# Performance work log

Hardware: AMD Instinct MI355X
Metric: run time of the kernel (lower is better)

Reference implementation:

```python
import jax, jax.numpy as jnp
import numpy as np

IN_F, OUT_F = 4096, 4096
IN_Q, OUT_Q = IN_F // 4, OUT_F // 4


def setup_inputs() -> dict:
    key = jax.random.key(0)
    kx, kr, ki, kj, kk = jax.random.split(key, 5)
    std = 1.0 / np.sqrt(IN_F)
    x = jax.random.normal(kx, (4, 2048, IN_F), dtype=jnp.float32)
    Wr = std * jax.random.normal(kr, (OUT_Q, IN_Q), dtype=jnp.float32)
    Wi = std * jax.random.normal(ki, (OUT_Q, IN_Q), dtype=jnp.float32)
    Wj = std * jax.random.normal(kj, (OUT_Q, IN_Q), dtype=jnp.float32)
    Wk = std * jax.random.normal(kk, (OUT_Q, IN_Q), dtype=jnp.float32)
    bias = jnp.zeros((OUT_F,), dtype=jnp.float32)
    return {"x": x, "Wr": Wr, "Wi": Wi, "Wj": Wj, "Wk": Wk, "bias": bias}


def _hamilton_block(Wr, Wi, Wj, Wk):
    # Assemble the structured [4*out_q, 4*in_q] Hamilton block weight so the
    # whole op is ONE large GEMM instead of 16 small ones (same math).
    row_r = jnp.concatenate([Wr, -Wi, -Wj, -Wk], axis=1)
    row_i = jnp.concatenate([Wi,  Wr,  Wk, -Wj], axis=1)
    row_j = jnp.concatenate([Wj, -Wk,  Wr,  Wi], axis=1)
    row_k = jnp.concatenate([Wk,  Wj, -Wi,  Wr], axis=1)
    return jnp.concatenate([row_r, row_i, row_j, row_k], axis=0)  # [OUT_F, IN_F]


def reference(x, Wr, Wi, Wj, Wk, bias):
    W = _hamilton_block(Wr, Wi, Wj, Wk)
    # x: [B, S, IN_F] @ W.T -> [B, S, OUT_F]
    out = jnp.einsum('bsf,of->bso', x, W) + bias
    return out
```

## Files before the change

### kernel.cpp

```cpp
#include <hip/hip_runtime.h>
#include <hip/hip_bf16.h>


#define M_DIM 8192
#define N_DIM 4096
#define K_DIM 4096
#define BK 64
#define NT (K_DIM / BK)

typedef __attribute__((ext_vector_type(8))) short bf16x8;
typedef __attribute__((ext_vector_type(4))) float f32x4;
typedef __attribute__((ext_vector_type(16))) float f32x16;
typedef __attribute__((ext_vector_type(8))) unsigned short ushort8;

static __device__ __forceinline__ unsigned short f2bf(float f) {
    unsigned int u = __float_as_uint(f);
    return (unsigned short)((u + 0x7fffu + ((u >> 16) & 1u)) >> 16);
}
static __device__ __forceinline__ unsigned short f2bf_sgn(float f, unsigned int sg) {
    unsigned int u = __float_as_uint(f) ^ sg;
    return (unsigned short)((u + 0x7fffu + ((u >> 16) & 1u)) >> 16);
}

__global__ __launch_bounds__(256) void cvt_x_kernel(const float* __restrict__ x,
                                                    unsigned short* __restrict__ xb) {
    int i = (blockIdx.x * 256 + threadIdx.x) * 8;
    f32x4 a = __builtin_nontemporal_load((const f32x4*)(x + i));
    f32x4 b = __builtin_nontemporal_load((const f32x4*)(x + i + 4));
    ushort8 o;
    o[0] = f2bf(a[0]); o[1] = f2bf(a[1]); o[2] = f2bf(a[2]); o[3] = f2bf(a[3]);
    o[4] = f2bf(b[0]); o[5] = f2bf(b[1]); o[6] = f2bf(b[2]); o[7] = f2bf(b[3]);
    *(ushort8*)(xb + i) = o;
}

__global__ __launch_bounds__(256) void prep_w_kernel(const float* __restrict__ Wr,
    const float* __restrict__ Wi, const float* __restrict__ Wj,
    const float* __restrict__ Wk, unsigned short* __restrict__ wb) {
    int row = blockIdx.x >> 1;
    int col = ((blockIdx.x & 1) * 256 + threadIdx.x) * 8;
    int p = row >> 10, q = col >> 10;
    int ci = p ^ q;
    const float* src = (ci == 0) ? Wr : (ci == 1) ? Wi : (ci == 2) ? Wj : Wk;
    unsigned int sg = ((0x428Eu >> (p * 4 + q)) & 1u) << 31;
    int so = (row & 1023) * 1024 + (col & 1023);
    f32x4 a = *(const f32x4*)(src + so);
    f32x4 b = *(const f32x4*)(src + so + 4);
    ushort8 o;
    o[0] = f2bf_sgn(a[0], sg); o[1] = f2bf_sgn(a[1], sg);
    o[2] = f2bf_sgn(a[2], sg); o[3] = f2bf_sgn(a[3], sg);
    o[4] = f2bf_sgn(b[0], sg); o[5] = f2bf_sgn(b[1], sg);
    o[6] = f2bf_sgn(b[2], sg); o[7] = f2bf_sgn(b[3], sg);
    *(ushort8*)(wb + row * 4096 + col) = o;
}

#define GLD16(gp, lp) __builtin_amdgcn_global_load_lds( \
    (const __attribute__((address_space(1))) void*)(gp), \
    (__attribute__((address_space(3))) void*)(lp), 16, 0, 0)

#define BAR() do { asm volatile("" ::: "memory"); \
                   __builtin_amdgcn_s_barrier(); \
                   asm volatile("" ::: "memory"); } while (0)
#define VM0() asm volatile("s_waitcnt vmcnt(0)" ::: "memory")
#define SB()  __builtin_amdgcn_sched_barrier(0)
#define LGKM(n) do { asm volatile("s_waitcnt lgkmcnt(" #n ")" ::: "memory"); SB(); } while (0)

#define DSR(dst, addr, imm) \
    asm volatile("ds_read_b128 %0, %1 offset:" imm : "=v"(dst) : "v"(addr))

#define MF32(a, b, c) __builtin_amdgcn_mfma_f32_32x32x16_bf16(a, b, c, 0, 0, 0)

#define DECL6(F) bf16x8 F##a0, F##a1, F##a2, F##a3, F##b0, F##b1
#define RD6(F, A0, A1, A2, A3, B0, B1) do { \
    DSR(F##a0, vA, A0); DSR(F##a1, vA, A1); DSR(F##a2, vA, A2); DSR(F##a3, vA, A3); \
    DSR(F##b0, vB, B0); DSR(F##b1, vB, B1); } while (0)

#define MFMA8(F) do { \
    __builtin_amdgcn_s_setprio(1); \
    acc[0][0] = MF32(F##a0, F##b0, acc[0][0]); \
    acc[0][1] = MF32(F##a0, F##b1, acc[0][1]); \
    acc[1][0] = MF32(F##a1, F##b0, acc[1][0]); \
    acc[1][1] = MF32(F##a1, F##b1, acc[1][1]); \
    acc[2][0] = MF32(F##a2, F##b0, acc[2][0]); \
    acc[2][1] = MF32(F##a2, F##b1, acc[2][1]); \
    acc[3][0] = MF32(F##a3, F##b0, acc[3][0]); \
    acc[3][1] = MF32(F##a3, F##b1, acc[3][1]); \
    __builtin_amdgcn_s_setprio(0); \
} while (0)

__global__ __launch_bounds__(512, 2) void qgemm_bf16(
    const unsigned short* __restrict__ A, const unsigned short* __restrict__ B,
    const float* __restrict__ bias, float* __restrict__ out)
{
    __shared__ __align__(16) unsigned short Lsh[65536];

    int bid = blockIdx.x;
    int cpx = gridDim.x >> 3;
    int wg  = (bid & 7) * cpx + (bid >> 3);
    int brow = (wg >> 4) * 256;
    int bcol = (wg & 15) * 256;

    int tid  = threadIdx.x;
    int lane = tid & 63;
    int wid  = tid >> 6;
    int wm   = wid >> 2;
    int wn   = wid & 3;
    int l31  = lane & 31;
    int hi   = lane >> 5;

    const unsigned short* Ag = A + (size_t)brow * K_DIM;
    const unsigned short* Bg = B + (size_t)bcol * K_DIM;

    unsigned lds0 = (unsigned)(size_t)(__attribute__((address_space(3))) void*)Lsh;
    unsigned vA = lds0 + (unsigned)(wm * 4096 + l31 * 32 + hi * 16);
    unsigned vB = lds0 + 32768u + (unsigned)(wn * 2048 + l31 * 32 + hi * 16);

    int soff[4];
    #pragma unroll
    for (int i = 0; i < 4; ++i) {
        int c = i * 512 + tid;
        soff[i] = ((c >> 1) & 255) * 4096 + (c >> 9) * 16 + (c & 1) * 8;
    }

    f32x16 acc[4][2] = {};

    auto STAGE = [&](int buf, int t) {
        const unsigned short* ga = Ag + t * BK;
        const unsigned short* gb = Bg + t * BK;
        char* l = (char*)Lsh + buf * 65536;
        #pragma unroll
        for (int i = 0; i < 4; ++i)
            GLD16(ga + soff[i], l + (i * 512 + tid) * 16);
        #pragma unroll
        for (int i = 0; i < 4; ++i)
            GLD16(gb + soff[i], l + 32768 + (i * 512 + tid) * 16);
    };

    STAGE(0, 0);
    VM0(); BAR();

    for (int t = 0; t < NT; ++t) {
        if (t + 1 < NT) STAGE((t & 1) ^ 1, t + 1);

        DECL6(f0); DECL6(f1); DECL6(f2); DECL6(f3);
        RD6(f0, "0", "1024", "2048", "3072", "0", "1024");
        RD6(f1, "8192", "9216", "10240", "11264", "8192", "9216");
        LGKM(6);
        MFMA8(f0);
        RD6(f2, "16384", "17408", "18432", "19456", "16384", "17408");
        LGKM(6);
        MFMA8(f1);
        RD6(f3, "24576", "25600", "26624", "27648", "24576", "25600");
        LGKM(6);
        MFMA8(f2);
        LGKM(0);
        MFMA8(f3);

        VM0();
        BAR();
        vA ^= 0x10000u; vB ^= 0x10000u;
    }

    #pragma unroll
    for (int ni = 0; ni < 2; ++ni) {
        int col = bcol + wn * 64 + ni * 32 + l31;
        float bv = bias[col];
        #pragma unroll
        for (int mi = 0; mi < 4; ++mi) {
            int r0 = brow + wm * 128 + mi * 32 + 4 * hi;
            #pragma unroll
            for (int r = 0; r < 16; ++r) {
                int row = r0 + (r & 3) + 8 * (r >> 2);
                __builtin_nontemporal_store(acc[mi][ni][r] + bv,
                                            &out[(size_t)row * N_DIM + col]);
            }
        }
    }
}

#define FBM 128
#define FBN 128
#define FBK 64
__global__ __launch_bounds__(256) void qgemm_fb(const float* __restrict__ x,
    const float* __restrict__ Wr, const float* __restrict__ Wi,
    const float* __restrict__ Wj, const float* __restrict__ Wk,
    const float* __restrict__ bias, float* __restrict__ out)
{
    __shared__ unsigned short As[FBM * FBK];
    __shared__ unsigned short Bs[FBN * FBK];

    int bid = blockIdx.x;
    int cpx = gridDim.x >> 3;
    int wg = (bid & 7) * cpx + (bid >> 3);
    int brow = (wg >> 5) * FBM;
    int bcol = (wg & 31) * FBN;

    int tid = threadIdx.x;
    int lane = tid & 63;
    int wv = tid >> 6;
    int wm = (wv >> 1) << 6;
    int wn = (wv & 1) << 6;
    int fr = lane & 15;
    int fk = (lane >> 4) << 3;

    int p = bcol >> 10;
    f32x4 acc[4][4] = {};

    for (int kt = 0; kt < K_DIM / FBK; ++kt) {
        int k0 = kt * FBK;
        int q = k0 >> 10;
        int ci = p ^ q;
        const float* wsrc = (ci == 0) ? Wr : (ci == 1) ? Wi : (ci == 2) ? Wj : Wk;
        unsigned int sg = ((0x428Eu >> (p * 4 + q)) & 1u) << 31;

        __syncthreads();
        #pragma unroll
        for (int i = 0; i < 4; ++i) {
            int c = i * 256 + tid;
            int row = c >> 3, colo = (c & 7) << 3;
            const float* s = x + (size_t)(brow + row) * K_DIM + k0 + colo;
            float4 a = *(const float4*)s;
            float4 b = *(const float4*)(s + 4);
            ushort8 o;
            o[0] = f2bf(a.x); o[1] = f2bf(a.y); o[2] = f2bf(a.z); o[3] = f2bf(a.w);
            o[4] = f2bf(b.x); o[5] = f2bf(b.y); o[6] = f2bf(b.z); o[7] = f2bf(b.w);
            *(ushort8*)(&As[c << 3]) = o;
        }
        #pragma unroll
        for (int i = 0; i < 4; ++i) {
            int c = i * 256 + tid;
            int row = c >> 3, colo = (c & 7) << 3;
            const float* s = wsrc + ((bcol + row) & 1023) * 1024 + ((k0 + colo) & 1023);
            float4 a = *(const float4*)s;
            float4 b = *(const float4*)(s + 4);
            ushort8 o;
            o[0] = f2bf_sgn(a.x, sg); o[1] = f2bf_sgn(a.y, sg);
            o[2] = f2bf_sgn(a.z, sg); o[3] = f2bf_sgn(a.w, sg);
            o[4] = f2bf_sgn(b.x, sg); o[5] = f2bf_sgn(b.y, sg);
            o[6] = f2bf_sgn(b.z, sg); o[7] = f2bf_sgn(b.w, sg);
            *(ushort8*)(&Bs[c << 3]) = o;
        }
        __syncthreads();

        #pragma unroll
        for (int ks = 0; ks < 2; ++ks) {
            bf16x8 af[4], bfr[4];
            #pragma unroll
            for (int m = 0; m < 4; ++m)
                af[m] = *(const bf16x8*)(&As[(wm + m * 16 + fr) * FBK + ks * 32 + fk]);
            #pragma unroll
            for (int n = 0; n < 4; ++n)
                bfr[n] = *(const bf16x8*)(&Bs[(wn + n * 16 + fr) * FBK + ks * 32 + fk]);
            #pragma unroll
            for (int m = 0; m < 4; ++m)
                #pragma unroll
                for (int n = 0; n < 4; ++n)
                    acc[m][n] = __builtin_amdgcn_mfma_f32_16x16x32_bf16(
                        af[m], bfr[n], acc[m][n], 0, 0, 0);
        }
    }

    int cr = (lane >> 4) << 2;
    int cc = lane & 15;
    #pragma unroll
    for (int n = 0; n < 4; ++n) {
        int col = bcol + wn + n * 16 + cc;
        float bv = bias[col];
        #pragma unroll
        for (int m = 0; m < 4; ++m) {
            int r0 = brow + wm + m * 16 + cr;
            #pragma unroll
            for (int r = 0; r < 4; ++r)
                out[(size_t)(r0 + r) * N_DIM + col] = acc[m][n][r] + bv;
        }
    }
}

extern "C" void kernel_launch(void* const* d_in, const int* in_sizes, int n_in,
                              void* d_out, int out_size, void* d_ws, size_t ws_size,
                              hipStream_t stream) {
    const float* x    = (const float*)d_in[0];
    const float* Wr   = (const float*)d_in[1];
    const float* Wi   = (const float*)d_in[2];
    const float* Wj   = (const float*)d_in[3];
    const float* Wk   = (const float*)d_in[4];
    const float* bias = (const float*)d_in[5];
    float* out = (float*)d_out;

    const size_t xb_bytes = (size_t)M_DIM * K_DIM * 2;
    const size_t wb_bytes = (size_t)N_DIM * K_DIM * 2;

    if (ws_size >= xb_bytes + wb_bytes) {
        unsigned short* xb = (unsigned short*)d_ws;
        unsigned short* wb = (unsigned short*)((char*)d_ws + xb_bytes);
        cvt_x_kernel<<<(M_DIM * K_DIM) / 2048, 256, 0, stream>>>(x, xb);
        prep_w_kernel<<<N_DIM * 2, 256, 0, stream>>>(Wr, Wi, Wj, Wk, wb);
        const int n_blocks = (M_DIM / 256) * (N_DIM / 256);
        qgemm_bf16<<<n_blocks, 512, 0, stream>>>(xb, wb, bias, out);
    } else {
        const int n_blocks = (M_DIM / FBM) * (N_DIM / FBN);
        qgemm_fb<<<n_blocks, 256, 0, stream>>>(x, Wr, Wi, Wj, Wk, bias, out);
    }
}
```

Baseline: 311.0 us.

## Switch LDS tile layout to row-major with XOR swizzle for conflict-free reads

Changes the shared-memory layout of the A and B tiles from a k-chunk-major arrangement to a row-major one (128 bytes per row), with 16-byte chunks XOR-swizzled by row index. Global-to-LDS load offsets and the per-lane ds_read addresses are recomputed to match, and the k-step is now selected by XORing the base address. The aim is to make global loads more contiguous per row and to cut LDS bank conflicts on the ds_read_b128 operand fetches. It adds per-read address XOR arithmetic, and the swizzle has to agree exactly on both the write and read sides.

```diff
diff --git a/kernel.cpp b/kernel.cpp
--- a/kernel.cpp
+++ b/kernel.cpp
@@ -70,9 +70,11 @@
 #define MF32(a, b, c) __builtin_amdgcn_mfma_f32_32x32x16_bf16(a, b, c, 0, 0, 0)
 
 #define DECL6(F) bf16x8 F##a0, F##a1, F##a2, F##a3, F##b0, F##b1
-#define RD6(F, A0, A1, A2, A3, B0, B1) do { \
-    DSR(F##a0, vA, A0); DSR(F##a1, vA, A1); DSR(F##a2, vA, A2); DSR(F##a3, vA, A3); \
-    DSR(F##b0, vB, B0); DSR(F##b1, vB, B1); } while (0)
+#define RD6(F, KX) do { \
+    unsigned aA_ = vA ^ (KX), aB_ = vB ^ (KX); \
+    DSR(F##a0, aA_, "0");     DSR(F##a1, aA_, "4096"); \
+    DSR(F##a2, aA_, "8192");  DSR(F##a3, aA_, "12288"); \
+    DSR(F##b0, aB_, "0");     DSR(F##b1, aB_, "4096"); } while (0)
 
 #define MFMA8(F) do { \
     __builtin_amdgcn_s_setprio(1); \
@@ -106,19 +108,23 @@
     int wn   = wid & 3;
     int l31  = lane & 31;
     int hi   = lane >> 5;
+    unsigned e0 = (unsigned)(l31 & 1);
+    unsigned e1 = (unsigned)((l31 >> 1) & 3);
 
     const unsigned short* Ag = A + (size_t)brow * K_DIM;
     const unsigned short* Bg = B + (size_t)bcol * K_DIM;
 
     unsigned lds0 = (unsigned)(size_t)(__attribute__((address_space(3))) void*)Lsh;
-    unsigned vA = lds0 + (unsigned)(wm * 4096 + l31 * 32 + hi * 16);
-    unsigned vB = lds0 + 32768u + (unsigned)(wn * 2048 + l31 * 32 + hi * 16);
+    unsigned vA = lds0 + (unsigned)(wm * 16384 + l31 * 128)
+                + (((unsigned)hi ^ e0) << 4) + (e1 << 5);
+    unsigned vB = lds0 + 32768u + (unsigned)(wn * 8192 + l31 * 128)
+                + (((unsigned)hi ^ e0) << 4) + (e1 << 5);
 
     int soff[4];
     #pragma unroll
     for (int i = 0; i < 4; ++i) {
         int c = i * 512 + tid;
-        soff[i] = ((c >> 1) & 255) * 4096 + (c >> 9) * 16 + (c & 1) * 8;
+        soff[i] = (c >> 3) * K_DIM + (((c & 7) ^ ((c >> 3) & 7)) << 3);
     }
 
     f32x16 acc[4][2] = {};
@@ -128,11 +134,10 @@
         const unsigned short* gb = Bg + t * BK;
         char* l = (char*)Lsh + buf * 65536;
         #pragma unroll
-        for (int i = 0; i < 4; ++i)
+        for (int i = 0; i < 4; ++i) {
             GLD16(ga + soff[i], l + (i * 512 + tid) * 16);
-        #pragma unroll
-        for (int i = 0; i < 4; ++i)
             GLD16(gb + soff[i], l + 32768 + (i * 512 + tid) * 16);
+        }
     };
 
     STAGE(0, 0);
@@ -142,14 +147,14 @@
         if (t + 1 < NT) STAGE((t & 1) ^ 1, t + 1);
 
         DECL6(f0); DECL6(f1); DECL6(f2); DECL6(f3);
-        RD6(f0, "0", "1024", "2048", "3072", "0", "1024");
-        RD6(f1, "8192", "9216", "10240", "11264", "8192", "9216");
+        RD6(f0, 0u);
+        RD6(f1, 32u);
         LGKM(6);
         MFMA8(f0);
-        RD6(f2, "16384", "17408", "18432", "19456", "16384", "17408");
+        RD6(f2, 64u);
         LGKM(6);
         MFMA8(f1);
-        RD6(f3, "24576", "25600", "26624", "27648", "24576", "25600");
+        RD6(f3, 96u);
         LGKM(6);
         MFMA8(f2);
         LGKM(0);
```

Measured after the change: 289.8 us. -6.8%, faster.

## Pre-swizzle X into MFMA fragment layout and load A directly to registers

Applied to the files above, without the earlier changes.

The X conversion kernel now transposes each 128x64 tile through shared memory and writes it into MFMA-operand order, so the GEMM can fetch A fragments straight into registers with global_load_dwordx4 and skip LDS for A. Only B is staged in LDS, now with an XOR swizzle and half the LDS footprint, and A loads run in a multi-stage register pipeline controlled by vmcnt waits. The goal is to cut LDS traffic and barrier pressure in the main loop. In exchange, A is no longer shared across waves: four waves reload the same A fragments from global/L2, which adds register pressure and global load traffic.

```diff
diff --git a/kernel.cpp b/kernel.cpp
--- a/kernel.cpp
+++ b/kernel.cpp
@@ -22,15 +22,31 @@
     return (unsigned short)((u + 0x7fffu + ((u >> 16) & 1u)) >> 16);
 }
 
-__global__ __launch_bounds__(256) void cvt_x_kernel(const float* __restrict__ x,
-                                                    unsigned short* __restrict__ xb) {
-    int i = (blockIdx.x * 256 + threadIdx.x) * 8;
-    f32x4 a = __builtin_nontemporal_load((const f32x4*)(x + i));
-    f32x4 b = __builtin_nontemporal_load((const f32x4*)(x + i + 4));
-    ushort8 o;
-    o[0] = f2bf(a[0]); o[1] = f2bf(a[1]); o[2] = f2bf(a[2]); o[3] = f2bf(a[3]);
-    o[4] = f2bf(b[0]); o[5] = f2bf(b[1]); o[6] = f2bf(b[2]); o[7] = f2bf(b[3]);
-    *(ushort8*)(xb + i) = o;
+__global__ __launch_bounds__(256) void cvt_x_t(const float* __restrict__ x,
+                                               unsigned short* __restrict__ xbt) {
+    __shared__ unsigned short T[128][72];
+    int bid = blockIdx.x;
+    int h = bid >> 6, t = bid & 63;
+    int tid = threadIdx.x;
+
+    #pragma unroll
+    for (int j = 0; j < 8; ++j) {
+        int c = j * 256 + tid;
+        int r = c >> 4, ko = (c & 15) * 4;
+        f32x4 v = __builtin_nontemporal_load(
+            (const f32x4*)(x + (size_t)(h * 128 + r) * 4096 + t * 64 + ko));
+        T[r][ko + 0] = f2bf(v[0]); T[r][ko + 1] = f2bf(v[1]);
+        T[r][ko + 2] = f2bf(v[2]); T[r][ko + 3] = f2bf(v[3]);
+    }
+    __syncthreads();
+    #pragma unroll
+    for (int i = 0; i < 4; ++i) {
+        int c = i * 256 + tid;
+        int ln = c & 63, mi = (c >> 6) & 3, kc = c >> 8;
+        int row = mi * 32 + (ln & 31), k = kc * 16 + (ln >> 5) * 8;
+        *(ushort8*)(xbt + (size_t)(h * 64 + t) * 8192 + (size_t)c * 8) =
+            *(const ushort8*)&T[row][k];
+    }
 }
 
 __global__ __launch_bounds__(256) void prep_w_kernel(const float* __restrict__ Wr,
@@ -60,113 +76,133 @@
 #define BAR() do { asm volatile("" ::: "memory"); \
                    __builtin_amdgcn_s_barrier(); \
                    asm volatile("" ::: "memory"); } while (0)
-#define VM0() asm volatile("s_waitcnt vmcnt(0)" ::: "memory")
 #define SB()  __builtin_amdgcn_sched_barrier(0)
-#define LGKM(n) do { asm volatile("s_waitcnt lgkmcnt(" #n ")" ::: "memory"); SB(); } while (0)
-
-#define DSR(dst, addr, imm) \
-    asm volatile("ds_read_b128 %0, %1 offset:" imm : "=v"(dst) : "v"(addr))
+#define VM(n) do { asm volatile("s_waitcnt vmcnt(" #n ")" ::: "memory"); SB(); } while (0)
 
 #define MF32(a, b, c) __builtin_amdgcn_mfma_f32_32x32x16_bf16(a, b, c, 0, 0, 0)
 
-#define DECL6(F) bf16x8 F##a0, F##a1, F##a2, F##a3, F##b0, F##b1
-#define RD6(F, A0, A1, A2, A3, B0, B1) do { \
-    DSR(F##a0, vA, A0); DSR(F##a1, vA, A1); DSR(F##a2, vA, A2); DSR(F##a3, vA, A3); \
-    DSR(F##b0, vB, B0); DSR(F##b1, vB, B1); } while (0)
-
-#define MFMA8(F) do { \
+#define ALOAD4(K, P) \
+    asm volatile("global_load_dwordx4 %0, %4, off\n\t" \
+                 "global_load_dwordx4 %1, %4, off offset:1024\n\t" \
+                 "global_load_dwordx4 %2, %4, off offset:2048\n\t" \
+                 "global_load_dwordx4 %3, %4, off offset:3072" \
+        : "=&v"(a##K##_0), "=&v"(a##K##_1), "=&v"(a##K##_2), "=&v"(a##K##_3) \
+        : "v"(P))
+
+#define MFMA8(A0, A1, A2, A3, B0, B1) do { \
     __builtin_amdgcn_s_setprio(1); \
-    acc[0][0] = MF32(F##a0, F##b0, acc[0][0]); \
-    acc[0][1] = MF32(F##a0, F##b1, acc[0][1]); \
-    acc[1][0] = MF32(F##a1, F##b0, acc[1][0]); \
-    acc[1][1] = MF32(F##a1, F##b1, acc[1][1]); \
-    acc[2][0] = MF32(F##a2, F##b0, acc[2][0]); \
-    acc[2][1] = MF32(F##a2, F##b1, acc[2][1]); \
-    acc[3][0] = MF32(F##a3, F##b0, acc[3][0]); \
-    acc[3][1] = MF32(F##a3, F##b1, acc[3][1]); \
+    acc[0][0] = MF32(A0, B0, acc[0][0]); acc[0][1] = MF32(A0, B1, acc[0][1]); \
+    acc[1][0] = MF32(A1, B0, acc[1][0]); acc[1][1] = MF32(A1, B1, acc[1][1]); \
+    acc[2][0] = MF32(A2, B0, acc[2][0]); acc[2][1] = MF32(A2, B1, acc[2][1]); \
+    acc[3][0] = MF32(A3, B0, acc[3][0]); acc[3][1] = MF32(A3, B1, acc[3][1]); \
     __builtin_amdgcn_s_setprio(0); \
+} while (0)
+
+#define BREAD(KC) \
+    bf16x8 b0 = *(const bf16x8*)(bb + (vB0 ^ ((KC) << 5))); \
+    bf16x8 b1 = *(const bf16x8*)(bb + (vB0 ^ ((KC) << 5)) + 4096)
+
+#define STAGEB(dstOff, tt) do { \
+    const unsigned short* gb_ = Bg + (tt) * BK; \
+    char* lb_ = (char*)Bsh + (dstOff); \
+    _Pragma("unroll") \
+    for (int i_ = 0; i_ < 4; ++i_) \
+        GLD16(gb_ + soffB[i_], lb_ + (i_ * 512 + tid) * 16); \
 } while (0)
 
 __global__ __launch_bounds__(512, 2) void qgemm_bf16(
     const unsigned short* __restrict__ A, const unsigned short* __restrict__ B,
     const float* __restrict__ bias, float* __restrict__ out)
 {
-    __shared__ __align__(16) unsigned short Lsh[65536];
+    __shared__ __align__(16) unsigned short Bsh[32768];
 
     int bid = blockIdx.x;
     int cpx = gridDim.x >> 3;
     int wg  = (bid & 7) * cpx + (bid >> 3);
-    int brow = (wg >> 4) * 256;
+    int mt   = wg >> 4;
     int bcol = (wg & 15) * 256;
 
     int tid  = threadIdx.x;
     int lane = tid & 63;
     int wid  = tid >> 6;
-    int wm   = wid >> 2;
+    int hA   = wid >> 2;
     int wn   = wid & 3;
     int l31  = lane & 31;
     int hi   = lane >> 5;
 
-    const unsigned short* Ag = A + (size_t)brow * K_DIM;
+    const char* pA0 = (const char*)A
+        + (size_t)((mt * 2 + hA) * 64) * 16384 + lane * 16;
+    const char* pA1 = pA0 + 4096;
+    const char* pA2 = pA0 + 8192;
+    const char* pA3 = pA0 + 12288;
+
     const unsigned short* Bg = B + (size_t)bcol * K_DIM;
-
-    unsigned lds0 = (unsigned)(size_t)(__attribute__((address_space(3))) void*)Lsh;
-    unsigned vA = lds0 + (unsigned)(wm * 4096 + l31 * 32 + hi * 16);
-    unsigned vB = lds0 + 32768u + (unsigned)(wn * 2048 + l31 * 32 + hi * 16);
-
-    int soff[4];
+    int soffB[4];
     #pragma unroll
     for (int i = 0; i < 4; ++i) {
         int c = i * 512 + tid;
-        soff[i] = ((c >> 1) & 255) * 4096 + (c >> 9) * 16 + (c & 1) * 8;
-    }
+        soffB[i] = (c >> 3) * K_DIM + (((c & 7) ^ ((c >> 3) & 7)) << 3);
+    }
+
+    unsigned vB0 = (unsigned)((wn * 64 + l31) * 128)
+                 + (((unsigned)hi ^ (unsigned)(l31 & 1)) << 4)
+                 + (((unsigned)(l31 >> 1) & 3u) << 5);
+    unsigned rb = 0;
 
     f32x16 acc[4][2] = {};
-
-    auto STAGE = [&](int buf, int t) {
-        const unsigned short* ga = Ag + t * BK;
-        const unsigned short* gb = Bg + t * BK;
-        char* l = (char*)Lsh + buf * 65536;
-        #pragma unroll
-        for (int i = 0; i < 4; ++i)
-            GLD16(ga + soff[i], l + (i * 512 + tid) * 16);
-        #pragma unroll
-        for (int i = 0; i < 4; ++i)
-            GLD16(gb + soff[i], l + 32768 + (i * 512 + tid) * 16);
-    };
-
-    STAGE(0, 0);
-    VM0(); BAR();
-
-    for (int t = 0; t < NT; ++t) {
-        if (t + 1 < NT) STAGE((t & 1) ^ 1, t + 1);
-
-        DECL6(f0); DECL6(f1); DECL6(f2); DECL6(f3);
-        RD6(f0, "0", "1024", "2048", "3072", "0", "1024");
-        RD6(f1, "8192", "9216", "10240", "11264", "8192", "9216");
-        LGKM(6);
-        MFMA8(f0);
-        RD6(f2, "16384", "17408", "18432", "19456", "16384", "17408");
-        LGKM(6);
-        MFMA8(f1);
-        RD6(f3, "24576", "25600", "26624", "27648", "24576", "25600");
-        LGKM(6);
-        MFMA8(f2);
-        LGKM(0);
-        MFMA8(f3);
-
-        VM0();
+    bf16x8 a0_0, a0_1, a0_2, a0_3;
+    bf16x8 a1_0, a1_1, a1_2, a1_3;
+    bf16x8 a2_0, a2_1, a2_2, a2_3;
+    bf16x8 a3_0, a3_1, a3_2, a3_3;
+
+    STAGEB(0, 0);
+    ALOAD4(0, pA0);
+    ALOAD4(1, pA1);
+
+    for (int t = 0; t < NT - 1; ++t) {
+        const char* bb = (const char*)Bsh + rb;
+        ALOAD4(2, pA2);
+        VM(8);
         BAR();
-        vA ^= 0x10000u; vB ^= 0x10000u;
-    }
-
+        { BREAD(0); MFMA8(a0_0, a0_1, a0_2, a0_3, b0, b1); }
+        ALOAD4(3, pA3);
+        STAGEB(rb ^ 0x8000u, t + 1);
+        VM(12);
+        { BREAD(1); MFMA8(a1_0, a1_1, a1_2, a1_3, b0, b1); }
+        pA0 += 16384;
+        ALOAD4(0, pA0);
+        VM(12);
+        { BREAD(2); MFMA8(a2_0, a2_1, a2_2, a2_3, b0, b1); }
+        pA1 += 16384;
+        ALOAD4(1, pA1);
+        pA2 += 16384; pA3 += 16384;
+        VM(12);
+        { BREAD(3); MFMA8(a3_0, a3_1, a3_2, a3_3, b0, b1); }
+        rb ^= 0x8000u;
+    }
+    {
+        const char* bb = (const char*)Bsh + rb;
+        ALOAD4(2, pA2);
+        VM(8);
+        BAR();
+        { BREAD(0); MFMA8(a0_0, a0_1, a0_2, a0_3, b0, b1); }
+        ALOAD4(3, pA3);
+        VM(8);
+        { BREAD(1); MFMA8(a1_0, a1_1, a1_2, a1_3, b0, b1); }
+        VM(4);
+        { BREAD(2); MFMA8(a2_0, a2_1, a2_2, a2_3, b0, b1); }
+        VM(0);
+        { BREAD(3); MFMA8(a3_0, a3_1, a3_2, a3_3, b0, b1); }
+    }
+
+    int brow = mt * 256;
     #pragma unroll
     for (int ni = 0; ni < 2; ++ni) {
         int col = bcol + wn * 64 + ni * 32 + l31;
         float bv = bias[col];
         #pragma unroll
         for (int mi = 0; mi < 4; ++mi) {
-            int r0 = brow + wm * 128 + mi * 32 + 4 * hi;
+            int r0 = brow + hA * 128 + mi * 32 + 4 * hi;
             #pragma unroll
             for (int r = 0; r < 16; ++r) {
                 int row = r0 + (r & 3) + 8 * (r >> 2);
@@ -290,12 +326,12 @@
     const size_t wb_bytes = (size_t)N_DIM * K_DIM * 2;
 
     if (ws_size >= xb_bytes + wb_bytes) {
-        unsigned short* xb = (unsigned short*)d_ws;
-        unsigned short* wb = (unsigned short*)((char*)d_ws + xb_bytes);
-        cvt_x_kernel<<<(M_DIM * K_DIM) / 2048, 256, 0, stream>>>(x, xb);
+        unsigned short* xbt = (unsigned short*)d_ws;
+        unsigned short* wb  = (unsigned short*)((char*)d_ws + xb_bytes);
+        cvt_x_t<<<64 * 64, 256, 0, stream>>>(x, xbt);
         prep_w_kernel<<<N_DIM * 2, 256, 0, stream>>>(Wr, Wi, Wj, Wk, wb);
         const int n_blocks = (M_DIM / 256) * (N_DIM / 256);
-        qgemm_bf16<<<n_blocks, 512, 0, stream>>>(xb, wb, bias, out);
+        qgemm_bf16<<<n_blocks, 512, 0, stream>>>(xbt, wb, bias, out);
     } else {
         const int n_blocks = (M_DIM / FBM) * (N_DIM / FBN);
         qgemm_fb<<<n_blocks, 256, 0, stream>>>(x, Wr, Wi, Wj, Wk, bias, out);
```

Result: faster. 291.3 us (-6.3%).

## Restructure bf16 GEMM main loop with swizzled LDS and split A/B prefetch

Applied to the files above, without the earlier changes.

Changes the LDS tile layout to row-major 128-byte rows with an XOR swizzle, which is meant to reduce ds_read bank conflicts. A and B halves are now loaded in separate stages, with B prefetched two iterations ahead and A one iteration ahead, interleaved with the MFMA clusters and a mid-iteration barrier. The hand-written inline asm ds_reads and explicit lgkmcnt waits are replaced by plain C++ loads, so instruction scheduling is left to the compiler. The partial vmcnt waits are intended to overlap global loads with compute. The cost is more complex buffer-reuse timing, which risks races and scheduling regressions.

```diff
diff --git a/kernel.cpp b/kernel.cpp
--- a/kernel.cpp
+++ b/kernel.cpp
@@ -60,38 +60,15 @@
 #define BAR() do { asm volatile("" ::: "memory"); \
                    __builtin_amdgcn_s_barrier(); \
                    asm volatile("" ::: "memory"); } while (0)
-#define VM0() asm volatile("s_waitcnt vmcnt(0)" ::: "memory")
-#define SB()  __builtin_amdgcn_sched_barrier(0)
-#define LGKM(n) do { asm volatile("s_waitcnt lgkmcnt(" #n ")" ::: "memory"); SB(); } while (0)
-
-#define DSR(dst, addr, imm) \
-    asm volatile("ds_read_b128 %0, %1 offset:" imm : "=v"(dst) : "v"(addr))
+#define VM(n) asm volatile("s_waitcnt vmcnt(" #n ")" ::: "memory")
 
 #define MF32(a, b, c) __builtin_amdgcn_mfma_f32_32x32x16_bf16(a, b, c, 0, 0, 0)
-
-#define DECL6(F) bf16x8 F##a0, F##a1, F##a2, F##a3, F##b0, F##b1
-#define RD6(F, A0, A1, A2, A3, B0, B1) do { \
-    DSR(F##a0, vA, A0); DSR(F##a1, vA, A1); DSR(F##a2, vA, A2); DSR(F##a3, vA, A3); \
-    DSR(F##b0, vB, B0); DSR(F##b1, vB, B1); } while (0)
-
-#define MFMA8(F) do { \
-    __builtin_amdgcn_s_setprio(1); \
-    acc[0][0] = MF32(F##a0, F##b0, acc[0][0]); \
-    acc[0][1] = MF32(F##a0, F##b1, acc[0][1]); \
-    acc[1][0] = MF32(F##a1, F##b0, acc[1][0]); \
-    acc[1][1] = MF32(F##a1, F##b1, acc[1][1]); \
-    acc[2][0] = MF32(F##a2, F##b0, acc[2][0]); \
-    acc[2][1] = MF32(F##a2, F##b1, acc[2][1]); \
-    acc[3][0] = MF32(F##a3, F##b0, acc[3][0]); \
-    acc[3][1] = MF32(F##a3, F##b1, acc[3][1]); \
-    __builtin_amdgcn_s_setprio(0); \
-} while (0)
 
 __global__ __launch_bounds__(512, 2) void qgemm_bf16(
     const unsigned short* __restrict__ A, const unsigned short* __restrict__ B,
     const float* __restrict__ bias, float* __restrict__ out)
 {
-    __shared__ __align__(16) unsigned short Lsh[65536];
+    __shared__ __align__(16) unsigned short Lsh[2][2][2][128 * 64];
 
     int bid = blockIdx.x;
     int cpx = gridDim.x >> 3;
@@ -102,63 +79,89 @@
     int tid  = threadIdx.x;
     int lane = tid & 63;
     int wid  = tid >> 6;
-    int wm   = wid >> 2;
+    int hA   = wid >> 2;
     int wn   = wid & 3;
+    int hB   = wn >> 1;
+    int rB0  = (wn & 1) << 6;
     int l31  = lane & 31;
     int hi   = lane >> 5;
 
     const unsigned short* Ag = A + (size_t)brow * K_DIM;
     const unsigned short* Bg = B + (size_t)bcol * K_DIM;
-
-    unsigned lds0 = (unsigned)(size_t)(__attribute__((address_space(3))) void*)Lsh;
-    unsigned vA = lds0 + (unsigned)(wm * 4096 + l31 * 32 + hi * 16);
-    unsigned vB = lds0 + 32768u + (unsigned)(wn * 2048 + l31 * 32 + hi * 16);
-
-    int soff[4];
-    #pragma unroll
-    for (int i = 0; i < 4; ++i) {
-        int c = i * 512 + tid;
-        soff[i] = ((c >> 1) & 255) * 4096 + (c >> 9) * 16 + (c & 1) * 8;
-    }
+    const char* LshB = (const char*)&Lsh[0][0][0][0];
+
+    unsigned inrow = (((unsigned)hi ^ (unsigned)(l31 & 1)) << 4)
+                   + (((unsigned)(l31 >> 1) & 3u) << 5);
+    unsigned oA = (unsigned)(hA * 16384 + l31 * 128) + inrow;
+    unsigned oB = 32768u + (unsigned)(hB * 16384 + (rB0 + l31) * 128) + inrow;
 
     f32x16 acc[4][2] = {};
 
-    auto STAGE = [&](int buf, int t) {
-        const unsigned short* ga = Ag + t * BK;
-        const unsigned short* gb = Bg + t * BK;
-        char* l = (char*)Lsh + buf * 65536;
-        #pragma unroll
-        for (int i = 0; i < 4; ++i)
-            GLD16(ga + soff[i], l + (i * 512 + tid) * 16);
-        #pragma unroll
-        for (int i = 0; i < 4; ++i)
-            GLD16(gb + soff[i], l + 32768 + (i * 512 + tid) * 16);
+    auto stage = [&](int buf, int ab, int half, int t) {
+        const unsigned short* g = (ab ? Bg : Ag) + (size_t)(half << 7) * K_DIM + t * BK;
+        unsigned short* l = &Lsh[buf][ab][half][0];
+        #pragma unroll
+        for (int i = 0; i < 2; ++i) {
+            int c = i * 512 + tid;
+            int r = c >> 3, s = c & 7;
+            GLD16(g + (size_t)r * K_DIM + ((s ^ (r & 7)) << 3), l + (c << 3));
+        }
     };
-
-    STAGE(0, 0);
-    VM0(); BAR();
+    auto RD = [&](unsigned off) -> bf16x8 {
+        return *(const bf16x8*)(LshB + off);
+    };
+
+#define CLUST(kc) do { \
+    __builtin_amdgcn_s_setprio(1); \
+    acc[0][0] = MF32(aF##kc##0, bA[kc], acc[0][0]); \
+    acc[0][1] = MF32(aF##kc##0, bB[kc], acc[0][1]); \
+    acc[1][0] = MF32(aF##kc##1, bA[kc], acc[1][0]); \
+    acc[1][1] = MF32(aF##kc##1, bB[kc], acc[1][1]); \
+    acc[2][0] = MF32(aF##kc##2, bA[kc], acc[2][0]); \
+    acc[2][1] = MF32(aF##kc##2, bB[kc], acc[2][1]); \
+    acc[3][0] = MF32(aF##kc##3, bA[kc], acc[3][0]); \
+    acc[3][1] = MF32(aF##kc##3, bB[kc], acc[3][1]); \
+    __builtin_amdgcn_s_setprio(0); \
+} while (0)
+
+#define RDA(kc) \
+    bf16x8 aF##kc##0 = RD((oA ^ ((unsigned)(kc) << 5))); \
+    bf16x8 aF##kc##1 = RD((oA ^ ((unsigned)(kc) << 5)) + 4096u); \
+    bf16x8 aF##kc##2 = RD((oA ^ ((unsigned)(kc) << 5)) + 8192u); \
+    bf16x8 aF##kc##3 = RD((oA ^ ((unsigned)(kc) << 5)) + 12288u)
+
+    stage(0, 0, 0, 0); stage(0, 0, 1, 0); stage(0, 1, 0, 0); stage(0, 1, 1, 0);
+    stage(1, 1, 0, 1); stage(1, 1, 1, 1);
+    VM(4); BAR();
 
     for (int t = 0; t < NT; ++t) {
-        if (t + 1 < NT) STAGE((t & 1) ^ 1, t + 1);
-
-        DECL6(f0); DECL6(f1); DECL6(f2); DECL6(f3);
-        RD6(f0, "0", "1024", "2048", "3072", "0", "1024");
-        RD6(f1, "8192", "9216", "10240", "11264", "8192", "9216");
-        LGKM(6);
-        MFMA8(f0);
-        RD6(f2, "16384", "17408", "18432", "19456", "16384", "17408");
-        LGKM(6);
-        MFMA8(f1);
-        RD6(f3, "24576", "25600", "26624", "27648", "24576", "25600");
-        LGKM(6);
-        MFMA8(f2);
-        LGKM(0);
-        MFMA8(f3);
-
-        VM0();
+        bf16x8 bA[4], bB[4];
+
+        #pragma unroll
+        for (int kc = 0; kc < 4; ++kc) {
+            unsigned ob = oB ^ ((unsigned)kc << 5);
+            bA[kc] = RD(ob);
+            bB[kc] = RD(ob + 4096u);
+        }
+        RDA(0);
+        if (t + 1 < NT) { stage((t & 1) ^ 1, 0, 0, t + 1); stage((t & 1) ^ 1, 0, 1, t + 1); }
+        RDA(1);
+        CLUST(0);
         BAR();
-        vA ^= 0x10000u; vB ^= 0x10000u;
-    }
+
+        if (t + 2 < NT) { stage(t & 1, 1, 0, t + 2); stage(t & 1, 1, 1, t + 2); }
+        RDA(2);
+        CLUST(1);
+        RDA(3);
+        CLUST(2);
+        CLUST(3);
+
+        if (t < NT - 2) { VM(4); } else { VM(0); }
+        BAR();
+        oA ^= 0x10000u; oB ^= 0x10000u;
+    }
+#undef CLUST
+#undef RDA
 
     #pragma unroll
     for (int ni = 0; ni < 2; ++ni) {
@@ -166,7 +169,7 @@
         float bv = bias[col];
         #pragma unroll
         for (int mi = 0; mi < 4; ++mi) {
-            int r0 = brow + wm * 128 + mi * 32 + 4 * hi;
+            int r0 = brow + hA * 128 + mi * 32 + 4 * hi;
             #pragma unroll
             for (int r = 0; r < 16; ++r) {
                 int row = r0 + (r & 3) + 8 * (r >> 2);
```

New measurement: 295.3 us. 1.05x faster.
